# Kernel optimization log

Measured on AMD Instinct MI355X. Metric: run time of the kernel, lower is better.

The kernel has to match this reference:

```python
import jax, jax.numpy as jnp
import numpy as np

SEQ, BATCH, HIDDEN = 2048, 1, 4096
NUM_HEADS, NUM_KV_HEADS, HEAD_DIM = 32, 8, 128
Q_PER_GROUP = NUM_HEADS // NUM_KV_HEADS  # 4
TOTAL_PROJ = NUM_KV_HEADS * (Q_PER_GROUP + 2) * HEAD_DIM  # 6144


def setup_inputs() -> dict:
    key = jax.random.key(0)
    k1, k2, k3 = jax.random.split(key, 3)
    tokens = jax.random.normal(k1, (SEQ, BATCH, HIDDEN), dtype=jnp.float32)
    # xavier-ish scaling so activations stay sane
    weight_qkv = jax.random.normal(k2, (TOTAL_PROJ, HIDDEN), dtype=jnp.float32) * (2.0 / (TOTAL_PROJ + HIDDEN)) ** 0.5
    weight_proj = jax.random.normal(k3, (HIDDEN, NUM_HEADS * HEAD_DIM), dtype=jnp.float32) * (2.0 / (HIDDEN + NUM_HEADS * HEAD_DIM)) ** 0.5
    return {"tokens": tokens, "weight_qkv": weight_qkv, "weight_proj": weight_proj}


def reference(tokens, weight_qkv, weight_proj):
    S, B, H = tokens.shape
    scale = 1.0 / HEAD_DIM ** 0.5
    # QKV projection with interleaved GQA layout: per KV group [q0..q_{g-1}, k, v]
    qkv = jnp.einsum('sbh,ph->sbp', tokens, weight_qkv)
    qkv = qkv.reshape(S, B, NUM_KV_HEADS, Q_PER_GROUP + 2, HEAD_DIM)
    q = qkv[:, :, :, :Q_PER_GROUP, :].reshape(S, B, NUM_HEADS, HEAD_DIM)
    k = qkv[:, :, :, Q_PER_GROUP, :]       # [S,B,KVH,D]
    v = qkv[:, :, :, Q_PER_GROUP + 1, :]
    # repeat_interleave KV heads to match Q heads (GQA)
    k = jnp.repeat(k, Q_PER_GROUP, axis=2)
    v = jnp.repeat(v, Q_PER_GROUP, axis=2)
    # [S,B,H,D] -> [B,H,S,D]
    q = q.transpose(1, 2, 0, 3)
    k = k.transpose(1, 2, 0, 3)
    v = v.transpose(1, 2, 0, 3)
    scores = jnp.einsum('bhsd,bhtd->bhst', q, k) * scale
    causal = jnp.tril(jnp.ones((S, S), dtype=bool))
    scores = jnp.where(causal, scores, jnp.finfo(scores.dtype).min)
    attn = jax.nn.softmax(scores, axis=-1)
    out = jnp.einsum('bhst,bhtd->bhsd', attn, v)
    # [B,H,S,D] -> [S,B,H*D]
    out = out.transpose(2, 0, 1, 3).reshape(S, B, NUM_HEADS * HEAD_DIM)
    return jnp.einsum('sbe,he->sbh', out, weight_proj)
```

## Files before the change

### kernel.cpp

```cpp
#include <hip/hip_runtime.h>
#include <hip/hip_bf16.h>
#include <stdint.h>

#define SEQ 2048
#define HIDDEN 4096
#define NHEADS 32
#define HD 128
#define QKV_LD 6144
#define OUT_LD 4096

typedef __attribute__((ext_vector_type(8))) short short8;
typedef __attribute__((ext_vector_type(4))) short short4v;
typedef __attribute__((ext_vector_type(4))) float f32x4;
typedef __attribute__((ext_vector_type(4))) int int4v;
typedef __attribute__((ext_vector_type(2))) unsigned int uint2v;
typedef __attribute__((ext_vector_type(4))) float float4v;

__device__ __forceinline__ short f2bf(float f) {
  uint32_t u = __builtin_bit_cast(uint32_t, f);
  u += 0x7fff + ((u >> 16) & 1);
  return (short)(u >> 16);
}

__global__ void cast_kernel(const float* __restrict__ in, short* __restrict__ out, int n4) {
  int stride = gridDim.x * blockDim.x;
  for (int i = blockIdx.x * blockDim.x + threadIdx.x; i < n4; i += stride) {
    float4v v = ((const float4v*)in)[i];
    short4v o;
    o[0] = f2bf(v[0]); o[1] = f2bf(v[1]); o[2] = f2bf(v[2]); o[3] = f2bf(v[3]);
    ((short4v*)out)[i] = o;
  }
}

template <typename OT, int NBF>
__global__ __launch_bounds__(512, 2) void gemm256b(const short* __restrict__ A,
                                                   const short* __restrict__ B,
                                                   OT* __restrict__ C,
                                                   int M, int N, int K, int NT) {
  __shared__ __align__(16) short lds[32768 + NBF * 8192];
  const int tid = threadIdx.x;
  const int w = tid >> 6, lane = tid & 63;
  const int wr = w >> 2, wc = w & 3;
  const int llo = lane & 15, lhi = lane >> 4;

  const int nwg = gridDim.x;
  const int cpx = nwg >> 3;
  const int work = ((int)blockIdx.x & 7) * cpx + ((int)blockIdx.x >> 3);
  const int mt = work / NT, nt = work % NT;
  const size_t arow0 = (size_t)mt * 256, brow0 = (size_t)nt * (NBF * 64);
  const short* Ab = A + arow0 * K;
  const short* Bb = B + brow0 * K;

  f32x4 acc[8][NBF] = {};

  auto STAGE_A = [&](int kt, int j) {
    const int bufd = kt & 1;
    const int r0 = (j << 6) + (w << 3);
    const int row = r0 + (lane >> 3);
    const short* src = Ab + (size_t)row * K + (kt << 6) + (((lane & 7) ^ (row & 7)) << 3);
    short* dst = lds + (bufd << 14) + r0 * 64;
    __builtin_amdgcn_global_load_lds(
        (const __attribute__((address_space(1))) uint32_t*)src,
        (__attribute__((address_space(3))) uint32_t*)dst, 16, 0, 0);
  };
  auto STAGE_B = [&](int kt, int j) {
    const int bufd = kt & 1;
    const int r0 = (j << 6) + (w << 3);
    const int row = r0 + (lane >> 3);
    const short* src = Bb + (size_t)row * K + (kt << 6) + (((lane & 7) ^ (row & 7)) << 3);
    short* dst = lds + 32768 + bufd * (NBF << 12) + r0 * 64;
    __builtin_amdgcn_global_load_lds(
        (const __attribute__((address_space(1))) uint32_t*)src,
        (__attribute__((address_space(3))) uint32_t*)dst, 16, 0, 0);
  };
  auto STAGE = [&](int kt) {
#pragma unroll
    for (int j = 0; j < 4; j++) STAGE_A(kt, j);
#pragma unroll
    for (int j = 0; j < NBF; j++) STAGE_B(kt, j);
  };

  auto LDA = [&](int bufd, int m, int kk) -> short8 {
    const int row = (wr << 7) + (m << 4) + llo;
    const int ch = ((kk << 2) + lhi) ^ (row & 7);
    return *(const short8*)(lds + (bufd << 14) + row * 64 + (ch << 3));
  };
  auto LDB = [&](int bufd, int n, int kk) -> short8 {
    const int row = wc * (NBF << 4) + (n << 4) + llo;
    const int ch = ((kk << 2) + lhi) ^ (row & 7);
    return *(const short8*)(lds + 32768 + bufd * (NBF << 12) + row * 64 + (ch << 3));
  };

  auto HALF = [&](int bufd, int ktStage, bool doStage, bool gateFinal) {
    short8 b_[NBF][2], a_[2][2], an_[2][2], an2_[2][2];
#pragma unroll
    for (int n = 0; n < NBF; n++) { b_[n][0] = LDB(bufd, n, 0); b_[n][1] = LDB(bufd, n, 1); }
#pragma unroll
    for (int mi = 0; mi < 2; mi++) { a_[mi][0] = LDA(bufd, mi, 0); a_[mi][1] = LDA(bufd, mi, 1); }
    __builtin_amdgcn_s_barrier();
    asm volatile("s_waitcnt lgkmcnt(0)" ::: "memory");
    __builtin_amdgcn_sched_barrier(0);
    __builtin_amdgcn_s_setprio(1);
#pragma unroll
    for (int mi = 0; mi < 2; mi++)
#pragma unroll
      for (int n = 0; n < NBF; n++)
#pragma unroll
        for (int kk = 0; kk < 2; kk++)
          acc[mi][n] = __builtin_amdgcn_mfma_f32_16x16x32_bf16(a_[mi][kk], b_[n][kk], acc[mi][n], 0, 0, 0);
    __builtin_amdgcn_s_setprio(0);
    __builtin_amdgcn_s_barrier();
#pragma unroll
    for (int mi = 0; mi < 2; mi++) {
      an_[mi][0] = LDA(bufd, 2 + mi, 0);  an_[mi][1] = LDA(bufd, 2 + mi, 1);
      an2_[mi][0] = LDA(bufd, 4 + mi, 0); an2_[mi][1] = LDA(bufd, 4 + mi, 1);
    }
    __builtin_amdgcn_s_barrier();
    asm volatile("s_waitcnt lgkmcnt(0)" ::: "memory");
    __builtin_amdgcn_sched_barrier(0);
    __builtin_amdgcn_s_setprio(1);
#pragma unroll
    for (int mi = 0; mi < 2; mi++)
#pragma unroll
      for (int n = 0; n < NBF; n++)
#pragma unroll
        for (int kk = 0; kk < 2; kk++)
          acc[2 + mi][n] = __builtin_amdgcn_mfma_f32_16x16x32_bf16(an_[mi][kk], b_[n][kk], acc[2 + mi][n], 0, 0, 0);
    __builtin_amdgcn_s_setprio(0);
    __builtin_amdgcn_s_barrier();
#pragma unroll
    for (int mi = 0; mi < 2; mi++) { a_[mi][0] = LDA(bufd, 6 + mi, 0); a_[mi][1] = LDA(bufd, 6 + mi, 1); }
    __builtin_amdgcn_s_barrier();
    asm volatile("s_waitcnt lgkmcnt(0)" ::: "memory");
    __builtin_amdgcn_sched_barrier(0);
    __builtin_amdgcn_s_setprio(1);
#pragma unroll
    for (int mi = 0; mi < 2; mi++)
#pragma unroll
      for (int n = 0; n < NBF; n++)
#pragma unroll
        for (int kk = 0; kk < 2; kk++)
          acc[4 + mi][n] = __builtin_amdgcn_mfma_f32_16x16x32_bf16(an2_[mi][kk], b_[n][kk], acc[4 + mi][n], 0, 0, 0);
    __builtin_amdgcn_s_setprio(0);
    __builtin_amdgcn_s_barrier();
    if (doStage) STAGE(ktStage);
    __builtin_amdgcn_s_barrier();
    __builtin_amdgcn_sched_barrier(0);
    __builtin_amdgcn_s_setprio(1);
#pragma unroll
    for (int mi = 0; mi < 2; mi++)
#pragma unroll
      for (int n = 0; n < NBF; n++)
#pragma unroll
        for (int kk = 0; kk < 2; kk++)
          acc[6 + mi][n] = __builtin_amdgcn_mfma_f32_16x16x32_bf16(a_[mi][kk], b_[n][kk], acc[6 + mi][n], 0, 0, 0);
    __builtin_amdgcn_s_setprio(0);
    if (doStage) {
      if constexpr (NBF == 3) asm volatile("s_waitcnt vmcnt(7)" ::: "memory");
      else                    asm volatile("s_waitcnt vmcnt(6)" ::: "memory");
    } else if (gateFinal) {
      asm volatile("s_waitcnt vmcnt(0)" ::: "memory");
    }
    __builtin_amdgcn_s_barrier();
  };

  STAGE(0);
  STAGE(1);
  if constexpr (NBF == 3) asm volatile("s_waitcnt vmcnt(7)" ::: "memory");
  else                    asm volatile("s_waitcnt vmcnt(6)" ::: "memory");
  __builtin_amdgcn_s_barrier();

  const int NIT = (K >> 6) >> 1;
  for (int it = 0; it < NIT; ++it) {
    const bool stN = (it + 1 < NIT);
    HALF(0, 2 * it + 2, stN, !stN);
    HALF(1, 2 * it + 3, stN, false);
  }

#pragma unroll
  for (int m = 0; m < 8; m++)
#pragma unroll
    for (int n = 0; n < NBF; n++)
#pragma unroll
      for (int r = 0; r < 4; r++) {
        const size_t row = arow0 + (wr << 7) + (m << 4) + (lhi << 2) + r;
        const size_t col = brow0 + wc * (NBF << 4) + (n << 4) + llo;
        const float v = acc[m][n][r];
        if constexpr (sizeof(OT) == 2) C[row * N + col] = f2bf(v);
        else                           C[row * N + col] = v;
      }
}

__global__ __launch_bounds__(256, 2) void attn_fwd(const short* __restrict__ qkv,
                                                   short* __restrict__ aout) {
  const int qt = gridDim.y - 1 - blockIdx.y;
  const int h = blockIdx.x;
  const int kvh = h >> 2, g = h & 3;
  const int tid = threadIdx.x;
  const int wave = tid >> 6, lane = tid & 63;
  const int lhi = lane >> 4, llo = lane & 15;

  __shared__ __align__(16) short Ksm[2][64 * 128];
  __shared__ __align__(16) short Vsm[2][64 * 128];
  __shared__ __align__(16) short Psm[4][16 * 72];

  const float scale = 0.08838834764831845f;

  const int qrow = qt * 64 + wave * 16 + llo;
  const short* qbase = qkv + (size_t)qrow * QKV_LD + (kvh * 6 + g) * HD;
  short8 qf[4];
#pragma unroll
  for (int kk = 0; kk < 4; kk++) qf[kk] = *(const short8*)(qbase + kk * 32 + lhi * 8);

  f32x4 o[8] = {};
  float mrow[4], lrow[4];
#pragma unroll
  for (int r = 0; r < 4; r++) { mrow[r] = -1e30f; lrow[r] = 0.f; }

  const short* Kg = qkv + (kvh * 6 + 4) * HD;
  const short* Vg = qkv + (kvh * 6 + 5) * HD;

  const int k_row = lhi;
  const int v_vr = tid >> 4, v_vc = tid & 15;

  auto STAGE_K = [&](int t, int buf) {
#pragma unroll
    for (int c = 0; c < 4; c++) {
      const int call = wave * 4 + c;
      const int row = call * 4 + k_row;
      const int sc = llo ^ (row & 7);
      __builtin_amdgcn_global_load_lds(
          (const __attribute__((address_space(1))) uint32_t*)(Kg + (size_t)(t * 64 + row) * QKV_LD + sc * 8),
          (__attribute__((address_space(3))) uint32_t*)(&Ksm[buf][0] + call * 512), 16, 0, 0);
    }
  };
  short8 vreg[4];
  auto LOAD_V = [&](int t) {
#pragma unroll
    for (int c = 0; c < 4; c++) {
      const int vr = c * 16 + v_vr;
      vreg[c] = *(const short8*)(Vg + (size_t)(t * 64 + vr) * QKV_LD + v_vc * 8);
    }
  };
  auto WRITE_V = [&](int buf) {
#pragma unroll
    for (int c = 0; c < 4; c++) {
      const int vr = c * 16 + v_vr;
      *(short8*)(&Vsm[buf][0] + ((vr >> 2) * 8 + (v_vc >> 1)) * 64 + (vr & 3) * 16 + (v_vc & 1) * 8) = vreg[c];
    }
  };

  const uint32_t vlane0 = (uint32_t)(uintptr_t)(__attribute__((address_space(3))) short*)(&Vsm[0][0])
                          + (uint32_t)(lhi * 2048 + llo * 8);

  STAGE_K(0, 0);
  LOAD_V(0);
  asm volatile("s_waitcnt vmcnt(0)" ::: "memory");
  WRITE_V(0);
  __syncthreads();

  const int ntiles = qt + 1;
  for (int t = 0; t < ntiles; t++) {
    const int cur = t & 1, nxt = cur ^ 1;
    const bool pf = (t + 1 < ntiles);
    if (pf) { STAGE_K(t + 1, nxt); LOAD_V(t + 1); }

    const short* Kc = &Ksm[cur][0];
    f32x4 s[4] = {};
#pragma unroll
    for (int n = 0; n < 4; n++) {
#pragma unroll
      for (int kk = 0; kk < 4; kk++) {
        const int krow = n * 16 + llo;
        const int ch = (kk * 4 + lhi) ^ (krow & 7);
        short8 kf = *(const short8*)(Kc + krow * 128 + ch * 8);
        s[n] = __builtin_amdgcn_mfma_f32_16x16x32_bf16(qf[kk], kf, s[n], 0, 0, 0);
      }
    }

    float sv[4][4];
    const bool diag = (t == qt);
#pragma unroll
    for (int n = 0; n < 4; n++)
#pragma unroll
      for (int r = 0; r < 4; r++) {
        float x = s[n][r] * scale;
        if (diag && (n * 16 + llo > wave * 16 + lhi * 4 + r)) x = -1e30f;
        sv[n][r] = x;
      }

    float rm4[4];
#pragma unroll
    for (int r = 0; r < 4; r++) {
      float rm = fmaxf(fmaxf(sv[0][r], sv[1][r]), fmaxf(sv[2][r], sv[3][r]));
#pragma unroll
      for (int msk = 1; msk < 16; msk <<= 1) rm = fmaxf(rm, __shfl_xor(rm, msk));
      rm4[r] = rm;
    }
    bool need = false;
#pragma unroll
    for (int r = 0; r < 4; r++) need = need || (rm4[r] > mrow[r] + 8.0f);
    if (__any(need)) {
#pragma unroll
      for (int r = 0; r < 4; r++) {
        const float mnew = fmaxf(mrow[r], rm4[r]);
        const float a = __expf(mrow[r] - mnew);
        mrow[r] = mnew;
        lrow[r] *= a;
#pragma unroll
        for (int nn = 0; nn < 8; nn++) o[nn][r] *= a;
      }
    }
#pragma unroll
    for (int r = 0; r < 4; r++) {
      float rs = 0.f;
#pragma unroll
      for (int n = 0; n < 4; n++) {
        float p = __expf(sv[n][r] - mrow[r]);
        sv[n][r] = p;
        rs += p;
      }
#pragma unroll
      for (int msk = 1; msk < 16; msk <<= 1) rs += __shfl_xor(rs, msk);
      lrow[r] += rs;
    }

    short* P = &Psm[wave][0];
#pragma unroll
    for (int n = 0; n < 4; n++)
#pragma unroll
      for (int r = 0; r < 4; r++)
        P[(lhi * 4 + r) * 72 + n * 16 + llo] = f2bf(sv[n][r]);

    short8 pa0 = *(const short8*)(P + llo * 72 + lhi * 8);
    short8 pa1 = *(const short8*)(P + llo * 72 + 32 + lhi * 8);
    const uint32_t vlane = vlane0 + (uint32_t)(cur * 16384);
#pragma unroll
    for (int ks = 0; ks < 2; ks++) {
      uint2v vr_[8][2];
#pragma unroll
      for (int nn = 0; nn < 8; nn++)
#pragma unroll
        for (int hh = 0; hh < 2; hh++) {
          uint32_t a = vlane + (uint32_t)(ks * 8192 + hh * 1024 + nn * 128);
          asm volatile("ds_read_b64_tr_b16 %0, %1" : "=v"(vr_[nn][hh]) : "v"(a));
        }
      asm volatile("s_waitcnt lgkmcnt(0)" ::: "memory");
      __builtin_amdgcn_sched_barrier(0);
      const short8 pa = ks ? pa1 : pa0;
#pragma unroll
      for (int nn = 0; nn < 8; nn++) {
        int4v tv;
        tv[0] = (int)vr_[nn][0][0]; tv[1] = (int)vr_[nn][0][1];
        tv[2] = (int)vr_[nn][1][0]; tv[3] = (int)vr_[nn][1][1];
        o[nn] = __builtin_amdgcn_mfma_f32_16x16x32_bf16(pa, __builtin_bit_cast(short8, tv), o[nn], 0, 0, 0);
      }
    }

    if (pf) {
      asm volatile("s_waitcnt vmcnt(0)" ::: "memory");
      __syncthreads();
      WRITE_V(nxt);
      __syncthreads();
    }
  }

#pragma unroll
  for (int nn = 0; nn < 8; nn++)
#pragma unroll
    for (int r = 0; r < 4; r++) {
      const size_t row = qt * 64 + wave * 16 + lhi * 4 + r;
      const size_t col = (size_t)h * HD + nn * 16 + llo;
      aout[row * OUT_LD + col] = f2bf(o[nn][r] / lrow[r]);
    }
}

extern "C" void kernel_launch(void* const* d_in, const int* in_sizes, int n_in,
                              void* d_out, int out_size, void* d_ws, size_t ws_size,
                              hipStream_t stream) {
  const float* tokens = (const float*)d_in[0];
  const float* wqkv   = (const float*)d_in[1];
  const float* wproj  = (const float*)d_in[2];
  float* out = (float*)d_out;

  short* tok_bf   = (short*)d_ws;
  short* wqkv_bf  = tok_bf   + (size_t)SEQ * HIDDEN;
  short* wproj_bf = wqkv_bf  + (size_t)QKV_LD * HIDDEN;
  short* qkv_bf   = wproj_bf + (size_t)HIDDEN * OUT_LD;
  short* attn_bf  = qkv_bf   + (size_t)SEQ * QKV_LD;

  cast_kernel<<<2048, 256, 0, stream>>>(tokens, tok_bf, SEQ * HIDDEN / 4);
  cast_kernel<<<2048, 256, 0, stream>>>(wqkv, wqkv_bf, QKV_LD * HIDDEN / 4);
  cast_kernel<<<2048, 256, 0, stream>>>(wproj, wproj_bf, HIDDEN * OUT_LD / 4);

  gemm256b<short, 3><<<256, 512, 0, stream>>>(tok_bf, wqkv_bf, qkv_bf, SEQ, QKV_LD, HIDDEN, QKV_LD / 192);

  attn_fwd<<<dim3(NHEADS, SEQ / 64), 256, 0, stream>>>(qkv_bf, attn_bf);

  gemm256b<float, 2><<<256, 512, 0, stream>>>(attn_bf, wproj_bf, out, SEQ, OUT_LD, HIDDEN, OUT_LD / 128);
}
```

Before: 338.9 us.

## Replace hand-scheduled ping-pong GEMM main loop with simple per-tile loop

```diff
diff --git a/kernel.cpp b/kernel.cpp
--- a/kernel.cpp
+++ b/kernel.cpp
@@ -91,90 +91,42 @@
     return *(const short8*)(lds + 32768 + bufd * (NBF << 12) + row * 64 + (ch << 3));
   };
 
-  auto HALF = [&](int bufd, int ktStage, bool doStage, bool gateFinal) {
-    short8 b_[NBF][2], a_[2][2], an_[2][2], an2_[2][2];
-#pragma unroll
-    for (int n = 0; n < NBF; n++) { b_[n][0] = LDB(bufd, n, 0); b_[n][1] = LDB(bufd, n, 1); }
-#pragma unroll
-    for (int mi = 0; mi < 2; mi++) { a_[mi][0] = LDA(bufd, mi, 0); a_[mi][1] = LDA(bufd, mi, 1); }
-    __builtin_amdgcn_s_barrier();
-    asm volatile("s_waitcnt lgkmcnt(0)" ::: "memory");
-    __builtin_amdgcn_sched_barrier(0);
-    __builtin_amdgcn_s_setprio(1);
-#pragma unroll
-    for (int mi = 0; mi < 2; mi++)
-#pragma unroll
-      for (int n = 0; n < NBF; n++)
-#pragma unroll
-        for (int kk = 0; kk < 2; kk++)
-          acc[mi][n] = __builtin_amdgcn_mfma_f32_16x16x32_bf16(a_[mi][kk], b_[n][kk], acc[mi][n], 0, 0, 0);
-    __builtin_amdgcn_s_setprio(0);
-    __builtin_amdgcn_s_barrier();
-#pragma unroll
-    for (int mi = 0; mi < 2; mi++) {
-      an_[mi][0] = LDA(bufd, 2 + mi, 0);  an_[mi][1] = LDA(bufd, 2 + mi, 1);
-      an2_[mi][0] = LDA(bufd, 4 + mi, 0); an2_[mi][1] = LDA(bufd, 4 + mi, 1);
-    }
-    __builtin_amdgcn_s_barrier();
-    asm volatile("s_waitcnt lgkmcnt(0)" ::: "memory");
-    __builtin_amdgcn_sched_barrier(0);
-    __builtin_amdgcn_s_setprio(1);
-#pragma unroll
-    for (int mi = 0; mi < 2; mi++)
-#pragma unroll
-      for (int n = 0; n < NBF; n++)
-#pragma unroll
-        for (int kk = 0; kk < 2; kk++)
-          acc[2 + mi][n] = __builtin_amdgcn_mfma_f32_16x16x32_bf16(an_[mi][kk], b_[n][kk], acc[2 + mi][n], 0, 0, 0);
-    __builtin_amdgcn_s_setprio(0);
-    __builtin_amdgcn_s_barrier();
-#pragma unroll
-    for (int mi = 0; mi < 2; mi++) { a_[mi][0] = LDA(bufd, 6 + mi, 0); a_[mi][1] = LDA(bufd, 6 + mi, 1); }
-    __builtin_amdgcn_s_barrier();
-    asm volatile("s_waitcnt lgkmcnt(0)" ::: "memory");
-    __builtin_amdgcn_sched_barrier(0);
-    __builtin_amdgcn_s_setprio(1);
-#pragma unroll
-    for (int mi = 0; mi < 2; mi++)
-#pragma unroll
-      for (int n = 0; n < NBF; n++)
-#pragma unroll
-        for (int kk = 0; kk < 2; kk++)
-          acc[4 + mi][n] = __builtin_amdgcn_mfma_f32_16x16x32_bf16(an2_[mi][kk], b_[n][kk], acc[4 + mi][n], 0, 0, 0);
-    __builtin_amdgcn_s_setprio(0);
-    __builtin_amdgcn_s_barrier();
-    if (doStage) STAGE(ktStage);
-    __builtin_amdgcn_s_barrier();
-    __builtin_amdgcn_sched_barrier(0);
-    __builtin_amdgcn_s_setprio(1);
-#pragma unroll
-    for (int mi = 0; mi < 2; mi++)
-#pragma unroll
-      for (int n = 0; n < NBF; n++)
-#pragma unroll
-        for (int kk = 0; kk < 2; kk++)
-          acc[6 + mi][n] = __builtin_amdgcn_mfma_f32_16x16x32_bf16(a_[mi][kk], b_[n][kk], acc[6 + mi][n], 0, 0, 0);
-    __builtin_amdgcn_s_setprio(0);
-    if (doStage) {
-      if constexpr (NBF == 3) asm volatile("s_waitcnt vmcnt(7)" ::: "memory");
-      else                    asm volatile("s_waitcnt vmcnt(6)" ::: "memory");
-    } else if (gateFinal) {
-      asm volatile("s_waitcnt vmcnt(0)" ::: "memory");
-    }
-    __builtin_amdgcn_s_barrier();
-  };
-
   STAGE(0);
   STAGE(1);
   if constexpr (NBF == 3) asm volatile("s_waitcnt vmcnt(7)" ::: "memory");
   else                    asm volatile("s_waitcnt vmcnt(6)" ::: "memory");
   __builtin_amdgcn_s_barrier();
 
-  const int NIT = (K >> 6) >> 1;
-  for (int it = 0; it < NIT; ++it) {
-    const bool stN = (it + 1 < NIT);
-    HALF(0, 2 * it + 2, stN, !stN);
-    HALF(1, 2 * it + 3, stN, false);
+  const int NKT = K >> 6;
+  for (int kt = 0; kt < NKT; ++kt) {
+    const int bufd = kt & 1;
+    short8 b_[NBF][2];
+#pragma unroll
+    for (int n = 0; n < NBF; n++) { b_[n][0] = LDB(bufd, n, 0); b_[n][1] = LDB(bufd, n, 1); }
+#pragma unroll
+    for (int m = 0; m < 8; m++) {
+      short8 a0 = LDA(bufd, m, 0);
+      short8 a1 = LDA(bufd, m, 1);
+      __builtin_amdgcn_s_setprio(1);
+#pragma unroll
+      for (int n = 0; n < NBF; n++) {
+        acc[m][n] = __builtin_amdgcn_mfma_f32_16x16x32_bf16(a0, b_[n][0], acc[m][n], 0, 0, 0);
+        acc[m][n] = __builtin_amdgcn_mfma_f32_16x16x32_bf16(a1, b_[n][1], acc[m][n], 0, 0, 0);
+      }
+      __builtin_amdgcn_s_setprio(0);
+    }
+    asm volatile("s_waitcnt lgkmcnt(0)" ::: "memory");
+    __builtin_amdgcn_s_barrier();
+    if (kt + 2 < NKT) STAGE(kt + 2);
+    if (kt + 1 < NKT) {
+      if (kt + 2 < NKT) {
+        if constexpr (NBF == 3) asm volatile("s_waitcnt vmcnt(7)" ::: "memory");
+        else                    asm volatile("s_waitcnt vmcnt(6)" ::: "memory");
+      } else {
+        asm volatile("s_waitcnt vmcnt(0)" ::: "memory");
+      }
+      __builtin_amdgcn_s_barrier();
+    }
   }
 
 #pragma unroll
```

New measurement: 333.7 us. About the same (-1.5%).
